# Performance work log

Measured on AMD Instinct MI355X. Metric: run time of the kernel, lower is better.

## Reference

```python
import jax, jax.numpy as jnp
import numpy as np
import math

B, S, D, H = 2, 2048, 2048, 16
HD = D // H  # head_dim = 128
NEG = -9e15


def setup_inputs() -> dict:
    key = jax.random.key(0)
    k1, k2, k3 = jax.random.split(key, 3)
    x = jax.random.normal(k1, (B, S, D), dtype=jnp.float32)
    Wqkv = jax.random.normal(k2, (D, 3 * D), dtype=jnp.float32) * (1.0 / math.sqrt(D))
    bqkv = jnp.zeros((3 * D,), dtype=jnp.float32)
    Wo = jax.random.normal(k3, (D, D), dtype=jnp.float32) * (1.0 / math.sqrt(D))
    bo = jnp.zeros((D,), dtype=jnp.float32)
    return {"x": x, "Wqkv": Wqkv, "bqkv": bqkv, "Wo": Wo, "bo": bo}


def reference(x, Wqkv, bqkv, Wo, bo):
    b, s, d = x.shape
    # fused QKV projection
    qkv = x @ Wqkv + bqkv                       # [B,S,3D]
    qkv = qkv.reshape(b, s, H, 3 * HD)          # per-head interleaved q|k|v
    qkv = qkv.transpose(0, 2, 1, 3)             # [B,H,S,3*HD]
    q, k, v = jnp.split(qkv, 3, axis=-1)        # each [B,H,S,HD]
    scale = 1.0 / math.sqrt(HD)
    logits = jnp.einsum('bhqd,bhkd->bhqk', q, k) * scale  # [B,H,S,S]
    causal = jnp.tril(jnp.ones((s, s), dtype=bool))[None, None]
    logits = jnp.where(causal, logits, NEG)
    score = jax.nn.softmax(logits, axis=-1)
    attn = jnp.einsum('bhqk,bhkd->bhqd', score, v)         # [B,H,S,HD]
    attn = attn.transpose(0, 2, 1, 3).reshape(b, s, d)
    return attn @ Wo + bo
```

## Files before the change

### kernel.cpp

```cpp
#include <hip/hip_runtime.h>
#include <stdint.h>

#define DEV static __device__ __forceinline__

typedef _Float16 half8 __attribute__((ext_vector_type(8)));
typedef _Float16 half4 __attribute__((ext_vector_type(4)));
typedef float f32x4 __attribute__((ext_vector_type(4)));
typedef uint16_t u16x8 __attribute__((ext_vector_type(8)));

constexpr int Bc = 2, Sc = 2048, Dc = 2048, Hc = 16, HDc = 128;
constexpr int D3c = 3 * Dc;
constexpr int Mc = Bc * Sc;

DEV void gl_lds16(const void* g, void* l) {
    __builtin_amdgcn_global_load_lds(
        (const __attribute__((address_space(1))) unsigned int*)g,
        (__attribute__((address_space(3))) unsigned int*)l,
        16, 0, 0);
}

__global__ __launch_bounds__(256) void cast_f16_kernel(
    const float* __restrict__ in, _Float16* __restrict__ out)
{
    int i = blockIdx.x * 256 + threadIdx.x;
    const float4* p = (const float4*)in;
    float4 a = p[i * 2], b = p[i * 2 + 1];
    half8 hv;
    hv[0] = (_Float16)a.x; hv[1] = (_Float16)a.y; hv[2] = (_Float16)a.z; hv[3] = (_Float16)a.w;
    hv[4] = (_Float16)b.x; hv[5] = (_Float16)b.y; hv[6] = (_Float16)b.z; hv[7] = (_Float16)b.w;
    *(half8*)(out + (size_t)i * 8) = hv;
}

__global__ __launch_bounds__(256) void transpose_cast_kernel(
    const float* __restrict__ in, _Float16* __restrict__ out, int R, int C)
{
    __shared__ float ls[64][64];
    const int t = threadIdx.x;
    const int r0 = blockIdx.y * 64, c0 = blockIdx.x * 64;
    {
        const int rr = t >> 4, lc = t & 15;
#pragma unroll
        for (int p = 0; p < 4; ++p) {
            int r = p * 16 + rr;
            int pc = lc ^ ((r >> 3) & 7);
            *(float4*)&ls[r][pc * 4] =
                *(const float4*)&in[(size_t)(r0 + r) * C + c0 + lc * 4];
        }
    }
    __syncthreads();
    {
        const int oc = t >> 3, ss = (t & 7) * 8;
#pragma unroll
        for (int p = 0; p < 2; ++p) {
            int c = p * 32 + oc;
            int lc = c >> 2, wi = c & 3;
            half8 hv;
#pragma unroll
            for (int j = 0; j < 8; ++j) {
                int r = ss + j;
                hv[j] = (_Float16)ls[r][(lc ^ ((r >> 3) & 7)) * 4 + wi];
            }
            *(half8*)&out[(size_t)(c0 + c) * R + r0 + ss] = hv;
        }
    }
}

__global__ __launch_bounds__(256) void transpose_v_kernel(
    const uint16_t* __restrict__ qkv, uint16_t* __restrict__ vt)
{
    __shared__ uint16_t ls[64][64];
    const int t = threadIdx.x;
    const int s0 = blockIdx.x * 64, d0 = blockIdx.y * 64, bh = blockIdx.z;
    const int b = bh >> 4, h = bh & 15;
    {
        const int sr = t >> 3, lc = t & 7;
#pragma unroll
        for (int p = 0; p < 2; ++p) {
            int s = p * 32 + sr;
            int pc = lc ^ ((s >> 3) & 7);
            *(u16x8*)&ls[s][pc * 8] =
                *(const u16x8*)&qkv[(size_t)(b * Sc + s0 + s) * D3c + h * 384 + 256 + d0 + lc * 8];
        }
    }
    __syncthreads();
    {
        const int od = t >> 3, ss = (t & 7) * 8;
#pragma unroll
        for (int p = 0; p < 2; ++p) {
            int d = p * 32 + od;
            int lc = d >> 3, wi = d & 7;
            u16x8 hv;
#pragma unroll
            for (int j = 0; j < 8; ++j) {
                int s = ss + j;
                hv[j] = ls[s][(lc ^ ((s >> 3) & 7)) * 8 + wi];
            }
            *(u16x8*)&vt[(size_t)(bh * HDc + d0 + d) * Sc + s0 + ss] = hv;
        }
    }
}

template <int BF16OUT>
__global__ __launch_bounds__(256, 2) void gemm_bt_kernel(
    const _Float16* __restrict__ A, const _Float16* __restrict__ Bt,
    const float* __restrict__ bias, void* __restrict__ Cout,
    int M, int N, int K)
{
    __shared__ __align__(16) char smem[32768];
    char* sA = smem;
    char* sB = smem + 16384;
    const int t = threadIdx.x, w = t >> 6, lane = t & 63;
    const int quad = lane >> 4, l15 = lane & 15;
    const int wr = w >> 1, wc = w & 1;
    const int n0 = blockIdx.x * 128, m0 = blockIdx.y * 128;

    const f32x4 vzero = {0.f, 0.f, 0.f, 0.f};
    f32x4 acc[4][4];
#pragma unroll
    for (int i = 0; i < 4; ++i)
#pragma unroll
        for (int j = 0; j < 4; ++j) acc[i][j] = vzero;

    const int kiters = K >> 6;
    for (int kk = 0; kk < kiters; ++kk) {
#pragma unroll
        for (int i = 0; i < 4; ++i) {
            int c = i * 256 + t;
            int row = c >> 3, kbs = c & 7, kact = kbs ^ (row & 7);
            gl_lds16(A + (size_t)(m0 + row) * K + kk * 64 + kact * 8,
                     sA + (i * 256 + w * 64) * 16);
        }
#pragma unroll
        for (int i = 0; i < 4; ++i) {
            int c = i * 256 + t;
            int row = c >> 3, kbs = c & 7, kact = kbs ^ (row & 7);
            gl_lds16(Bt + (size_t)(n0 + row) * K + kk * 64 + kact * 8,
                     sB + (i * 256 + w * 64) * 16);
        }
        __syncthreads();
#pragma unroll
        for (int ks = 0; ks < 2; ++ks) {
            half8 af[4], bf[4];
#pragma unroll
            for (int mt = 0; mt < 4; ++mt) {
                int row = wr * 64 + mt * 16 + l15;
                int kact = (ks * 4 + quad) ^ (l15 & 7);
                af[mt] = *(const half8*)(sA + row * 128 + kact * 16);
            }
#pragma unroll
            for (int nt = 0; nt < 4; ++nt) {
                int row = wc * 64 + nt * 16 + l15;
                int kact = (ks * 4 + quad) ^ (l15 & 7);
                bf[nt] = *(const half8*)(sB + row * 128 + kact * 16);
            }
#pragma unroll
            for (int mt = 0; mt < 4; ++mt)
#pragma unroll
                for (int nt = 0; nt < 4; ++nt)
                    acc[mt][nt] = __builtin_amdgcn_mfma_f32_16x16x32_f16(
                        af[mt], bf[nt], acc[mt][nt], 0, 0, 0);
        }
        __syncthreads();
    }

#pragma unroll
    for (int nt = 0; nt < 4; ++nt) {
        int col = n0 + wc * 64 + nt * 16 + l15;
        float bv = bias[col];
#pragma unroll
        for (int mt = 0; mt < 4; ++mt)
#pragma unroll
            for (int r = 0; r < 4; ++r) {
                int row = m0 + wr * 64 + mt * 16 + quad * 4 + r;
                float v = acc[mt][nt][r] + bv;
                if (BF16OUT) ((_Float16*)Cout)[(size_t)row * N + col] = (_Float16)v;
                else         ((float*)Cout)[(size_t)row * N + col] = v;
            }
    }
}

__global__ __launch_bounds__(256, 4) void flash_kernel(
    const _Float16* __restrict__ qkv, const _Float16* __restrict__ vt,
    _Float16* __restrict__ attn)
{
    __shared__ __align__(16) char smem[32768];
    char* sK = smem;
    char* sV = smem + 16384;

    const int t = threadIdx.x, w = t >> 6, lane = t & 63;
    const int quad = lane >> 4, l15 = lane & 15;
    const int bh = blockIdx.x;
    const int qt = 31 - blockIdx.y;
    const int b = bh >> 4, h = bh & 15;
    const int q0 = qt * 64;
    const int qrow = q0 + w * 16 + l15;

    half8 qf[4];
#pragma unroll
    for (int ks = 0; ks < 4; ++ks) {
        const _Float16* p = qkv + (size_t)(b * Sc + qrow) * D3c +
                            h * 384 + ks * 32 + quad * 8;
        qf[ks] = *(const half8*)p;
    }

    const f32x4 vzero = {0.f, 0.f, 0.f, 0.f};
    f32x4 o[8];
#pragma unroll
    for (int dt = 0; dt < 8; ++dt) o[dt] = vzero;
    float m_st = -1e30f, l_st = 0.f;

    const float kScale = 0.08838834764831845f * 1.4426950408889634f;
    const int nkt = qt + 1;

    for (int kt = 0; kt < nkt; ++kt) {
#pragma unroll
        for (int i = 0; i < 4; ++i) {
            int c = i * 256 + t;
            int row = c >> 4, kbs = c & 15, kact = kbs ^ (row & 15);
            gl_lds16(qkv + (size_t)(b * Sc + kt * 64 + row) * D3c + h * 384 + 128 + kact * 8,
                     sK + (i * 256 + w * 64) * 16);
        }
#pragma unroll
        for (int i = 0; i < 4; ++i) {
            int c = i * 256 + t;
            int row = c >> 3, kbs = c & 7, kact = kbs ^ (row & 7);
            gl_lds16(vt + (size_t)(bh * HDc + row) * Sc + kt * 64 + kact * 8,
                     sV + (i * 256 + w * 64) * 16);
        }
        __syncthreads();

        f32x4 sf[4];
#pragma unroll
        for (int kb = 0; kb < 4; ++kb) sf[kb] = vzero;
        __builtin_amdgcn_s_setprio(1);
#pragma unroll
        for (int ks = 0; ks < 4; ++ks) {
#pragma unroll
            for (int kb = 0; kb < 4; ++kb) {
                int row = kb * 16 + l15;
                int slot = (ks * 4 + quad) ^ l15;
                half8 kf = *(const half8*)(sK + row * 256 + slot * 16);
                sf[kb] = __builtin_amdgcn_mfma_f32_16x16x32_f16(kf, qf[ks], sf[kb], 0, 0, 0);
            }
        }
        __builtin_amdgcn_s_setprio(0);

        const bool domask = (kt == qt);
        float rm = -1e30f;
#pragma unroll
        for (int kb = 0; kb < 4; ++kb)
#pragma unroll
            for (int r = 0; r < 4; ++r) {
                float v = sf[kb][r] * kScale;
                if (domask) {
                    int col = kt * 64 + kb * 16 + quad * 4 + r;
                    if (col > qrow) v = -1e30f;
                }
                sf[kb][r] = v;
                rm = fmaxf(rm, v);
            }
        rm = fmaxf(rm, __shfl_xor(rm, 16, 64));
        rm = fmaxf(rm, __shfl_xor(rm, 32, 64));
        float mn = fmaxf(m_st, rm);
        float alpha = __builtin_amdgcn_exp2f(m_st - mn);
        m_st = mn;

        half4 pb[4];
        float rs = 0.f;
#pragma unroll
        for (int kb = 0; kb < 4; ++kb)
#pragma unroll
            for (int r = 0; r < 4; ++r) {
                float p = __builtin_amdgcn_exp2f(sf[kb][r] - mn);
                rs += p;
                pb[kb][r] = (_Float16)p;
            }
        rs += __shfl_xor(rs, 16, 64);
        rs += __shfl_xor(rs, 32, 64);
        l_st = l_st * alpha + rs;

#pragma unroll
        for (int dt = 0; dt < 8; ++dt)
#pragma unroll
            for (int r = 0; r < 4; ++r) o[dt][r] *= alpha;

        __builtin_amdgcn_s_setprio(1);
#pragma unroll
        for (int kb = 0; kb < 4; ++kb) {
#pragma unroll
            for (int dt = 0; dt < 8; ++dt) {
                int row = dt * 16 + l15;
                int slot = (kb * 2 + (quad >> 1)) ^ (l15 & 7);
                half4 vf = *(const half4*)(sV + row * 128 + slot * 16 + (quad & 1) * 8);
                o[dt] = __builtin_amdgcn_mfma_f32_16x16x16f16(vf, pb[kb], o[dt], 0, 0, 0);
            }
        }
        __builtin_amdgcn_s_setprio(0);
        __syncthreads();
    }

    char* sO = smem;
    float linv = 1.0f / l_st;
#pragma unroll
    for (int dt = 0; dt < 8; ++dt) {
        half4 hv;
#pragma unroll
        for (int r = 0; r < 4; ++r) hv[r] = (_Float16)(o[dt][r] * linv);
        *(half4*)(sO + (w * 16 + l15) * 272 + (dt * 16 + quad * 4) * 2) = hv;
    }
    __syncthreads();
#pragma unroll
    for (int i = 0; i < 4; ++i) {
        int q = i * 16 + (t >> 4);
        int d = (t & 15) * 8;
        half8 hv = *(const half8*)(sO + q * 272 + d * 2);
        *(half8*)(attn + (size_t)(b * Sc + q0 + q) * Dc + h * HDc + d) = hv;
    }
}

extern "C" void kernel_launch(void* const* d_in, const int* in_sizes, int n_in,
                              void* d_out, int out_size, void* d_ws, size_t ws_size,
                              hipStream_t stream)
{
    (void)in_sizes; (void)n_in; (void)out_size; (void)ws_size;
    const float* x    = (const float*)d_in[0];
    const float* Wqkv = (const float*)d_in[1];
    const float* bqkv = (const float*)d_in[2];
    const float* Wo   = (const float*)d_in[3];
    const float* bo   = (const float*)d_in[4];
    float* out = (float*)d_out;

    _Float16* xb  = (_Float16*)d_ws;
    _Float16* wt1 = xb  + (size_t)Mc * Dc;
    _Float16* wt2 = wt1 + (size_t)D3c * Dc;
    _Float16* qkv = wt2 + (size_t)Dc * Dc;
    _Float16* vtg  = wt1;
    _Float16* attn = xb;

    cast_f16_kernel<<<Mc * Dc / 2048, 256, 0, stream>>>(x, xb);
    transpose_cast_kernel<<<dim3(D3c / 64, Dc / 64), 256, 0, stream>>>(Wqkv, wt1, Dc, D3c);
    transpose_cast_kernel<<<dim3(Dc / 64, Dc / 64), 256, 0, stream>>>(Wo, wt2, Dc, Dc);
    gemm_bt_kernel<1><<<dim3(D3c / 128, Mc / 128), 256, 0, stream>>>(
        xb, wt1, bqkv, qkv, Mc, D3c, Dc);
    transpose_v_kernel<<<dim3(Sc / 64, 2, Bc * Hc), 256, 0, stream>>>(
        (const uint16_t*)qkv, (uint16_t*)vtg);
    flash_kernel<<<dim3(Bc * Hc, 32), 256, 0, stream>>>(qkv, vtg, attn);
    gemm_bt_kernel<0><<<dim3(Dc / 128, Mc / 128), 256, 0, stream>>>(
        attn, wt2, bo, out, Mc, Dc, Dc);
}
```

Before: 386.5 us.

## Merge prep kernels and enlarge flash attention query tile to 128 rows

Replaces the cast and two transpose-cast launches with a single prep kernel that dispatches work by block id, which removes launch overhead. The flash kernel now uses 512 threads (8 waves) per block covering 128 query rows, so each K/V tile loaded into LDS is shared by twice as many queries. Blocks are ordered with a zigzag so heavy and light causal tiles interleave. It also removes the s_setprio hints and raises the LDS size, which may lower occupancy.

Measured after the change: 360.4 us. 6.7% less time.

```diff
diff --git a/kernel.cpp b/kernel.cpp
--- a/kernel.cpp
+++ b/kernel.cpp
@@ -19,24 +19,11 @@
         16, 0, 0);
 }
 
-__global__ __launch_bounds__(256) void cast_f16_kernel(
-    const float* __restrict__ in, _Float16* __restrict__ out)
-{
-    int i = blockIdx.x * 256 + threadIdx.x;
-    const float4* p = (const float4*)in;
-    float4 a = p[i * 2], b = p[i * 2 + 1];
-    half8 hv;
-    hv[0] = (_Float16)a.x; hv[1] = (_Float16)a.y; hv[2] = (_Float16)a.z; hv[3] = (_Float16)a.w;
-    hv[4] = (_Float16)b.x; hv[5] = (_Float16)b.y; hv[6] = (_Float16)b.z; hv[7] = (_Float16)b.w;
-    *(half8*)(out + (size_t)i * 8) = hv;
-}
-
-__global__ __launch_bounds__(256) void transpose_cast_kernel(
-    const float* __restrict__ in, _Float16* __restrict__ out, int R, int C)
+DEV void transpose_tile(const float* __restrict__ in, _Float16* __restrict__ out,
+                        int R, int C, int bx, int by, int t)
 {
     __shared__ float ls[64][64];
-    const int t = threadIdx.x;
-    const int r0 = blockIdx.y * 64, c0 = blockIdx.x * 64;
+    const int r0 = by * 64, c0 = bx * 64;
     {
         const int rr = t >> 4, lc = t & 15;
 #pragma unroll
@@ -62,6 +49,30 @@
             }
             *(half8*)&out[(size_t)(c0 + c) * R + r0 + ss] = hv;
         }
+    }
+}
+
+__global__ __launch_bounds__(256) void prep_kernel(
+    const float* __restrict__ x, const float* __restrict__ Wqkv,
+    const float* __restrict__ Wo,
+    _Float16* __restrict__ xb, _Float16* __restrict__ wt1,
+    _Float16* __restrict__ wt2)
+{
+    const int id = blockIdx.x, t = threadIdx.x;
+    if (id < 4096) {
+        int i = id * 256 + t;
+        const float4* p = (const float4*)x;
+        float4 a = p[i * 2], b = p[i * 2 + 1];
+        half8 hv;
+        hv[0] = (_Float16)a.x; hv[1] = (_Float16)a.y; hv[2] = (_Float16)a.z; hv[3] = (_Float16)a.w;
+        hv[4] = (_Float16)b.x; hv[5] = (_Float16)b.y; hv[6] = (_Float16)b.z; hv[7] = (_Float16)b.w;
+        *(half8*)(xb + (size_t)i * 8) = hv;
+    } else if (id < 4096 + 3072) {
+        int id2 = id - 4096;
+        transpose_tile(Wqkv, wt1, Dc, D3c, id2 % 96, id2 / 96, t);
+    } else {
+        int id3 = id - 7168;
+        transpose_tile(Wo, wt2, Dc, Dc, id3 & 31, id3 >> 5, t);
     }
 }
 
@@ -179,20 +190,21 @@
     }
 }
 
-__global__ __launch_bounds__(256, 4) void flash_kernel(
+__global__ __launch_bounds__(512, 4) void flash_kernel(
     const _Float16* __restrict__ qkv, const _Float16* __restrict__ vt,
     _Float16* __restrict__ attn)
 {
-    __shared__ __align__(16) char smem[32768];
+    __shared__ __align__(16) char smem[36864];
     char* sK = smem;
     char* sV = smem + 16384;
 
     const int t = threadIdx.x, w = t >> 6, lane = t & 63;
     const int quad = lane >> 4, l15 = lane & 15;
     const int bh = blockIdx.x;
-    const int qt = 31 - blockIdx.y;
+    const int by = blockIdx.y;
+    const int qt = (by < 8) ? 15 - by : by - 8;
     const int b = bh >> 4, h = bh & 15;
-    const int q0 = qt * 64;
+    const int q0 = qt * 128;
     const int qrow = q0 + w * 16 + l15;
 
     half8 qf[4];
@@ -210,29 +222,28 @@
     float m_st = -1e30f, l_st = 0.f;
 
     const float kScale = 0.08838834764831845f * 1.4426950408889634f;
-    const int nkt = qt + 1;
+    const int nkt = 2 * qt + 2;
 
     for (int kt = 0; kt < nkt; ++kt) {
 #pragma unroll
-        for (int i = 0; i < 4; ++i) {
-            int c = i * 256 + t;
+        for (int i = 0; i < 2; ++i) {
+            int c = i * 512 + t;
             int row = c >> 4, kbs = c & 15, kact = kbs ^ (row & 15);
             gl_lds16(qkv + (size_t)(b * Sc + kt * 64 + row) * D3c + h * 384 + 128 + kact * 8,
-                     sK + (i * 256 + w * 64) * 16);
-        }
-#pragma unroll
-        for (int i = 0; i < 4; ++i) {
-            int c = i * 256 + t;
+                     sK + (i * 512 + w * 64) * 16);
+        }
+#pragma unroll
+        for (int i = 0; i < 2; ++i) {
+            int c = i * 512 + t;
             int row = c >> 3, kbs = c & 7, kact = kbs ^ (row & 7);
             gl_lds16(vt + (size_t)(bh * HDc + row) * Sc + kt * 64 + kact * 8,
-                     sV + (i * 256 + w * 64) * 16);
+                     sV + (i * 512 + w * 64) * 16);
         }
         __syncthreads();
 
         f32x4 sf[4];
 #pragma unroll
         for (int kb = 0; kb < 4; ++kb) sf[kb] = vzero;
-        __builtin_amdgcn_s_setprio(1);
 #pragma unroll
         for (int ks = 0; ks < 4; ++ks) {
 #pragma unroll
@@ -243,9 +254,8 @@
                 sf[kb] = __builtin_amdgcn_mfma_f32_16x16x32_f16(kf, qf[ks], sf[kb], 0, 0, 0);
             }
         }
-        __builtin_amdgcn_s_setprio(0);
-
-        const bool domask = (kt == qt);
+
+        const bool domask = (kt >= 2 * qt);
         float rm = -1e30f;
 #pragma unroll
         for (int kb = 0; kb < 4; ++kb)
@@ -284,7 +294,6 @@
 #pragma unroll
             for (int r = 0; r < 4; ++r) o[dt][r] *= alpha;
 
-        __builtin_amdgcn_s_setprio(1);
 #pragma unroll
         for (int kb = 0; kb < 4; ++kb) {
 #pragma unroll
@@ -295,7 +304,6 @@
                 o[dt] = __builtin_amdgcn_mfma_f32_16x16x16f16(vf, pb[kb], o[dt], 0, 0, 0);
             }
         }
-        __builtin_amdgcn_s_setprio(0);
         __syncthreads();
     }
 
@@ -311,7 +319,7 @@
     __syncthreads();
 #pragma unroll
     for (int i = 0; i < 4; ++i) {
-        int q = i * 16 + (t >> 4);
+        int q = i * 32 + (t >> 4);
         int d = (t & 15) * 8;
         half8 hv = *(const half8*)(sO + q * 272 + d * 2);
         *(half8*)(attn + (size_t)(b * Sc + q0 + q) * Dc + h * HDc + d) = hv;
@@ -337,14 +345,12 @@
     _Float16* vtg  = wt1;
     _Float16* attn = xb;
 
-    cast_f16_kernel<<<Mc * Dc / 2048, 256, 0, stream>>>(x, xb);
-    transpose_cast_kernel<<<dim3(D3c / 64, Dc / 64), 256, 0, stream>>>(Wqkv, wt1, Dc, D3c);
-    transpose_cast_kernel<<<dim3(Dc / 64, Dc / 64), 256, 0, stream>>>(Wo, wt2, Dc, Dc);
+    prep_kernel<<<8192, 256, 0, stream>>>(x, Wqkv, Wo, xb, wt1, wt2);
     gemm_bt_kernel<1><<<dim3(D3c / 128, Mc / 128), 256, 0, stream>>>(
         xb, wt1, bqkv, qkv, Mc, D3c, Dc);
     transpose_v_kernel<<<dim3(Sc / 64, 2, Bc * Hc), 256, 0, stream>>>(
         (const uint16_t*)qkv, (uint16_t*)vtg);
-    flash_kernel<<<dim3(Bc * Hc, 32), 256, 0, stream>>>(qkv, vtg, attn);
+    flash_kernel<<<dim3(Bc * Hc, 16), 512, 0, stream>>>(qkv, vtg, attn);
     gemm_bt_kernel<0><<<dim3(Dc / 128, Mc / 128), 256, 0, stream>>>(
         attn, wt2, bo, out, Mc, Dc, Dc);
 }
```
